# Kernel tuning notes

Hardware: AMD Instinct MI355X
Metric: run time of the kernel (lower is better)

Reference implementation:

```python
import jax, jax.numpy as jnp
import numpy as np

N = 25000   # nodes
E = 600000  # edges (multiple of 48)
IN, H, OUT = 128, 256, 128
SLOPE = 0.01  # LeakyReLU default negative_slope


def _lin(x, w, b):
    return x @ w.T + b


def _leaky(v):
    return jnp.where(v > 0, v, SLOPE * v)


def _sage(x, src, dst, lw, lb, rw):
    # PyG SAGEConv (aggr='mean', root_weight=True, normalize=False):
    # out = lin_l(mean_{j in N(i)} x_j) + lin_r(x_i)
    agg = jax.ops.segment_sum(x[src], dst, num_segments=N)
    deg = jax.ops.segment_sum(jnp.ones((src.shape[0],), x.dtype), dst, num_segments=N)
    mean = agg / jnp.maximum(deg, 1.0)[:, None]
    return mean @ lw.T + lb + x @ rw.T


def setup_inputs() -> dict:
    key = jax.random.key(0)
    ks = jax.random.split(key, 32)

    def w(k, o, i):
        return jax.random.normal(k, (o, i), jnp.float32) * (1.0 / np.sqrt(i))

    def b(k, o):
        return jax.random.normal(k, (o,), jnp.float32) * 0.01

    inp = {
        'x': jax.random.normal(ks[0], (N, IN), jnp.float32),
        'edge_index': jax.random.randint(ks[1], (2, E), 0, N, dtype=jnp.int32),
        'edge_attr': jax.random.normal(ks[2], (E, 1), jnp.float32),
        'batch': jnp.zeros((N,), jnp.int32),
        'prelin_w': w(ks[3], H, IN), 'prelin_b': b(ks[4], H),
        'conv1_lw': w(ks[5], H, H), 'conv1_lb': b(ks[6], H), 'conv1_rw': w(ks[7], H, H),
        'conv2_lw': w(ks[8], H, H), 'conv2_lb': b(ks[9], H), 'conv2_rw': w(ks[10], H, H),
        'conv3_lw': w(ks[11], OUT, H), 'conv3_lb': b(ks[12], OUT), 'conv3_rw': w(ks[13], OUT, H),
        'hh1_w': w(ks[14], H, H), 'hh1_b': b(ks[15], H),
        'hh2_w': w(ks[16], H, H), 'hh2_b': b(ks[17], H),
        'oo_w': w(ks[18], OUT, OUT), 'oo_b': b(ks[19], OUT),
        'lin96_w': w(ks[20], 1, 192), 'lin96_b': b(ks[21], 1),
        'lin32_w': w(ks[22], 1, 64), 'lin32_b': b(ks[23], 1),
    }
    return inp


def reference(x, edge_index, edge_attr, batch,
              prelin_w, prelin_b,
              conv1_lw, conv1_lb, conv1_rw,
              conv2_lw, conv2_lb, conv2_rw,
              conv3_lw, conv3_lb, conv3_rw,
              hh1_w, hh1_b, hh2_w, hh2_b,
              oo_w, oo_b, lin96_w, lin96_b, lin32_w, lin32_b):
    src, dst = edge_index[0], edge_index[1]
    h = jax.nn.relu(_lin(x, prelin_w, prelin_b))
    h = jax.nn.relu(_sage(h, src, dst, conv1_lw, conv1_lb, conv1_rw))
    h = _leaky(_lin(h, hh1_w, hh1_b))
    h = jax.nn.relu(_sage(h, src, dst, conv2_lw, conv2_lb, conv2_rw))
    h = _leaky(_lin(h, hh2_w, hh2_b))
    h = jax.nn.relu(_sage(h, src, dst, conv3_lw, conv3_lb, conv3_rw))
    h = _leaky(_lin(h, oo_w, oo_b))  # [N, 128]

    xl = h[src]  # edge_left  = edge_index[0]
    xr = h[dst]  # edge_right = edge_index[1]
    f96 = jnp.concatenate([xl[:, :96], xr[:, :96]], axis=1)  # [E, 192]
    f32 = jnp.concatenate([xl[:, 96:], xr[:, 96:]], axis=1)  # [E, 64]
    f96 = jax.nn.relu(_lin(f96, lin96_w, lin96_b))  # [E, 1]
    f32 = jax.nn.relu(_lin(f32, lin32_w, lin32_b))  # [E, 1]
    edge_out = f96 * edge_attr + f32                # [E, 1]
    edge_out = edge_out.reshape(-1, 48).mean(axis=1).reshape(-1, 1)  # [E/48, 1]
    return edge_out
```

## Files before the change

kernel.cpp:

```cpp
#include <hip/hip_runtime.h>
#include <hip/hip_bf16.h>

#define N_NODES 25000
#define N_EDGES 600000
#define ACT_NONE 0
#define ACT_RELU 1
#define ACT_LEAKY 2

typedef __bf16 bf16x8 __attribute__((ext_vector_type(8)));
typedef float f32x4 __attribute__((ext_vector_type(4)));
typedef unsigned short u16x8 __attribute__((ext_vector_type(8)));
typedef unsigned short u16x4 __attribute__((ext_vector_type(4)));
typedef short s16x4 __attribute__((ext_vector_type(4)));

__device__ __forceinline__ unsigned short f2bf(float x) {
    union { float f; unsigned int u; } v; v.f = x;
    unsigned int r = (v.u + 0x7fffu + ((v.u >> 16) & 1u)) >> 16;
    return (unsigned short)r;
}
__device__ __forceinline__ float bf2f(unsigned short b) {
    union { float f; unsigned int u; } v; v.u = ((unsigned int)b) << 16;
    return v.f;
}

__global__ __launch_bounds__(256) void hist_kernel(const int* __restrict__ dst,
                                                   int* __restrict__ deg, int E) {
    int e = blockIdx.x * 256 + threadIdx.x;
    if (e < E) atomicAdd(&deg[dst[e]], 1);
}

__global__ __launch_bounds__(1024) void scan_kernel(const int* __restrict__ deg,
                                                    int* __restrict__ off,
                                                    int* __restrict__ cursor, int n) {
    __shared__ int wsum[16];
    int t = threadIdx.x, w = t >> 6, l = t & 63;
    int carry = 0;
    for (int base = 0; base < n; base += 1024) {
        int v = (base + t < n) ? deg[base + t] : 0;
        int x = v;
        #pragma unroll
        for (int d = 1; d < 64; d <<= 1) {
            int y = __shfl_up(x, d);
            if (l >= d) x += y;
        }
        if (l == 63) wsum[w] = x;
        __syncthreads();
        if (w == 0 && l < 16) {
            int s = wsum[l];
            #pragma unroll
            for (int d = 1; d < 16; d <<= 1) {
                int y = __shfl_up(s, d);
                if (l >= d) s += y;
            }
            wsum[l] = s;
        }
        __syncthreads();
        int woff = (w > 0) ? wsum[w - 1] : 0;
        int excl = x + woff - v;
        if (base + t < n) {
            off[base + t] = carry + excl;
            cursor[base + t] = carry + excl;
        }
        int total = wsum[15];
        __syncthreads();
        carry += total;
    }
    if (t == 0) off[n] = carry;
}

__global__ __launch_bounds__(256) void scatter_kernel(const int* __restrict__ src,
                                                      const int* __restrict__ dst,
                                                      int* __restrict__ cursor,
                                                      int* __restrict__ csr_src, int E) {
    int e = blockIdx.x * 256 + threadIdx.x;
    if (e < E) {
        int d = dst[e];
        int pos = atomicAdd(&cursor[d], 1);
        csr_src[pos] = src[e];
    }
}

__global__ __launch_bounds__(256) void convert_kernel(const float* __restrict__ src,
                                                      unsigned short* __restrict__ hi,
                                                      unsigned short* __restrict__ lo, int n) {
    int i = blockIdx.x * 256 + threadIdx.x;
    if (i < n) {
        float x = src[i];
        unsigned short h = f2bf(x);
        hi[i] = h;
        lo[i] = f2bf(x - bf2f(h));
    }
}

struct CvtBatch {
    const float* src[10];
    unsigned short* hi[10];
    unsigned short* lo[10];
    int count[10];
};
__global__ __launch_bounds__(256) void convert_batch_kernel(CvtBatch b) {
    int seg = blockIdx.y;
    int n = b.count[seg];
    int i = blockIdx.x * 256 + threadIdx.x;
    if (i >= n) return;
    float x = b.src[seg][i];
    unsigned short h = f2bf(x);
    b.hi[seg][i] = h;
    b.lo[seg][i] = f2bf(x - bf2f(h));
}

__global__ __launch_bounds__(256) void sage_mean_kernel(const short* __restrict__ qt,
                                                        const float* __restrict__ qs4,
                                                        const int* __restrict__ off,
                                                        const int* __restrict__ csr_src,
                                                        unsigned short* __restrict__ mh,
                                                        unsigned short* __restrict__ ml) {
    int node = blockIdx.x * 4 + (threadIdx.x >> 6);
    if (node >= N_NODES) return;
    int lane = threadIdx.x & 63;
    int qidx = lane >> 4;
    int s0 = off[node], s1 = off[node + 1];
    f32x4 acc0 = {0.f, 0.f, 0.f, 0.f}, acc1 = {0.f, 0.f, 0.f, 0.f};
    f32x4 acc2 = {0.f, 0.f, 0.f, 0.f}, acc3 = {0.f, 0.f, 0.f, 0.f};
    long loff = (long)lane * 4;
    int e = s0;
    for (; e + 4 <= s1; e += 4) {
        int iA = csr_src[e], iB = csr_src[e + 1], iC = csr_src[e + 2], iD = csr_src[e + 3];
        s16x4 qa = *(const s16x4*)&qt[(long)iA * 256 + loff];
        s16x4 qb = *(const s16x4*)&qt[(long)iB * 256 + loff];
        s16x4 qc = *(const s16x4*)&qt[(long)iC * 256 + loff];
        s16x4 qd = *(const s16x4*)&qt[(long)iD * 256 + loff];
        float sa = qs4[(long)iA * 4 + qidx], sb = qs4[(long)iB * 4 + qidx];
        float sc = qs4[(long)iC * 4 + qidx], sd = qs4[(long)iD * 4 + qidx];
        #pragma unroll
        for (int j = 0; j < 4; ++j) {
            acc0[j] += sa * (float)qa[j];
            acc1[j] += sb * (float)qb[j];
            acc2[j] += sc * (float)qc[j];
            acc3[j] += sd * (float)qd[j];
        }
    }
    for (; e < s1; ++e) {
        int iA = csr_src[e];
        s16x4 qa = *(const s16x4*)&qt[(long)iA * 256 + loff];
        float sa = qs4[(long)iA * 4 + qidx];
        #pragma unroll
        for (int j = 0; j < 4; ++j) acc0[j] += sa * (float)qa[j];
    }
    float inv = 1.0f / fmaxf((float)(s1 - s0), 1.0f);
    f32x4 m = ((acc0 + acc1) + (acc2 + acc3)) * inv;
    u16x4 hb, lb;
    #pragma unroll
    for (int j = 0; j < 4; ++j) {
        unsigned short hv = f2bf(m[j]);
        hb[j] = hv;
        lb[j] = f2bf(m[j] - bf2f(hv));
    }
    long base = (long)node * 256 + loff;
    *(u16x4*)&mh[base] = hb;
    *(u16x4*)&ml[base] = lb;
}

__global__ __launch_bounds__(256, 2) void gemm_mfma_kernel(
    const unsigned short* __restrict__ A1h, const unsigned short* __restrict__ A1l,
    const unsigned short* __restrict__ W1h, const unsigned short* __restrict__ W1l,
    const unsigned short* __restrict__ A2h, const unsigned short* __restrict__ A2l,
    const unsigned short* __restrict__ W2h, const unsigned short* __restrict__ W2l,
    const float* __restrict__ bias,
    float* __restrict__ Cf, unsigned short* __restrict__ Ch, unsigned short* __restrict__ Cl,
    short* __restrict__ Cq, float* __restrict__ Cqs,
    const float* __restrict__ w96d, const float* __restrict__ w32d,
    float* __restrict__ nodeDotG,
    int M, int K, int O, int act)
{
    __shared__ unsigned short sAh[128][64];
    __shared__ unsigned short sAl[128][64];
    __shared__ unsigned short sWh[128][64];
    __shared__ unsigned short sWl[128][64];

    int tid = threadIdx.x;
    int row0 = blockIdx.x * 128;
    int col0 = blockIdx.y * 128;
    int wid = tid >> 6, lane = tid & 63;
    int wm = (wid >> 1) * 64, wo = (wid & 1) * 64;
    int fr = lane & 15, qk = lane >> 4;
    int rr = lane >> 3, qq = lane & 7;
    int shalf = (qq >> 2) * 32, scq = qq & 3;

    const int nt1 = K >> 6;
    const int nt  = (A2h != nullptr) ? (nt1 << 1) : nt1;

    f32x4 acc[4][4] = {};

    for (int t = 0; t < nt; ++t) {
        const unsigned short *Ah, *Al, *Wh, *Wl;
        int k0;
        if (t < nt1) { Ah = A1h; Al = A1l; Wh = W1h; Wl = W1l; k0 = t << 6; }
        else         { Ah = A2h; Al = A2l; Wh = W2h; Wl = W2l; k0 = (t - nt1) << 6; }

        #pragma unroll
        for (int i = 0; i < 4; ++i) {
            int rb = wid * 32 + i * 8;
            int r  = rb + rr;
            int gs = shalf + ((scq + (r >> 1)) & 3) * 8;
            long ar = (long)(row0 + r); if (ar > M - 1) ar = M - 1;
            long wr = (long)(col0 + r);
            __builtin_amdgcn_global_load_lds(
                (const __attribute__((address_space(1))) unsigned int*)(Ah + ar * K + k0 + gs),
                (__attribute__((address_space(3))) unsigned int*)&sAh[rb][0], 16, 0, 0);
            __builtin_amdgcn_global_load_lds(
                (const __attribute__((address_space(1))) unsigned int*)(Al + ar * K + k0 + gs),
                (__attribute__((address_space(3))) unsigned int*)&sAl[rb][0], 16, 0, 0);
            __builtin_amdgcn_global_load_lds(
                (const __attribute__((address_space(1))) unsigned int*)(Wh + wr * K + k0 + gs),
                (__attribute__((address_space(3))) unsigned int*)&sWh[rb][0], 16, 0, 0);
            __builtin_amdgcn_global_load_lds(
                (const __attribute__((address_space(1))) unsigned int*)(Wl + wr * K + k0 + gs),
                (__attribute__((address_space(3))) unsigned int*)&sWl[rb][0], 16, 0, 0);
        }
        __syncthreads();

        #pragma unroll
        for (int kk = 0; kk < 2; ++kk) {
            bf16x8 ah[4], al[4], bh[4], bl[4];
            #pragma unroll
            for (int i = 0; i < 4; ++i) {
                int rowA = wm + i * 16 + fr;
                int offA = rowA * 64 + kk * 32 + 8 * ((qk - (rowA >> 1)) & 3);
                ah[i] = *(const bf16x8*)(&sAh[0][0] + offA);
                al[i] = *(const bf16x8*)(&sAl[0][0] + offA);
                int rowB = wo + i * 16 + fr;
                int offB = rowB * 64 + kk * 32 + 8 * ((qk - (rowB >> 1)) & 3);
                bh[i] = *(const bf16x8*)(&sWh[0][0] + offB);
                bl[i] = *(const bf16x8*)(&sWl[0][0] + offB);
            }
            #pragma unroll
            for (int i = 0; i < 4; ++i) {
                #pragma unroll
                for (int j = 0; j < 4; ++j) {
                    acc[i][j] = __builtin_amdgcn_mfma_f32_16x16x32_bf16(ah[i], bh[j], acc[i][j], 0, 0, 0);
                    acc[i][j] = __builtin_amdgcn_mfma_f32_16x16x32_bf16(ah[i], bl[j], acc[i][j], 0, 0, 0);
                    acc[i][j] = __builtin_amdgcn_mfma_f32_16x16x32_bf16(al[i], bh[j], acc[i][j], 0, 0, 0);
                }
            }
        }
        __syncthreads();
    }

    int rgrp = (lane >> 4) * 4;
    int cl_ = lane & 15;
    int quarter = (col0 + wo) >> 6;

    float wa96[4], wb96[4], wa32[4], wb32[4];
    if (nodeDotG) {
        #pragma unroll
        for (int j = 0; j < 4; ++j) {
            int c = wo + j * 16 + cl_;
            bool lo96 = c < 96;
            wa96[j] = lo96 ? w96d[c] : 0.0f;
            wb96[j] = lo96 ? w96d[96 + c] : 0.0f;
            wa32[j] = lo96 ? 0.0f : w32d[c - 96];
            wb32[j] = lo96 ? 0.0f : w32d[c - 64];
        }
    }

    #pragma unroll
    for (int i = 0; i < 4; ++i) {
        float bv[4];
        #pragma unroll
        for (int j = 0; j < 4; ++j) bv[j] = bias[col0 + wo + j * 16 + cl_];
        #pragma unroll
        for (int r = 0; r < 4; ++r) {
            int grow = row0 + wm + i * 16 + rgrp + r;
            float vv[4];
            float m = 0.0f;
            #pragma unroll
            for (int j = 0; j < 4; ++j) {
                float v = acc[i][j][r] + bv[j];
                if (act == ACT_RELU)       v = fmaxf(v, 0.0f);
                else if (act == ACT_LEAKY) v = (v > 0.0f) ? v : 0.01f * v;
                vv[j] = v;
                m = fmaxf(m, fabsf(v));
            }
            float qinv = 0.0f;
            if (Cq) {
                #pragma unroll
                for (int d = 1; d < 16; d <<= 1) m = fmaxf(m, __shfl_xor(m, d));
                qinv = (m > 0.0f) ? 32767.0f / m : 0.0f;
            }
            bool ok = grow < M;
            #pragma unroll
            for (int j = 0; j < 4; ++j) {
                int gcol = col0 + wo + j * 16 + cl_;
                long idx = (long)grow * O + gcol;
                if (ok) {
                    float v = vv[j];
                    if (Cf) Cf[idx] = v;
                    if (Ch) {
                        unsigned short hbits = f2bf(v);
                        Ch[idx] = hbits;
                        Cl[idx] = f2bf(v - bf2f(hbits));
                    }
                    if (Cq) Cq[idx] = (short)(int)rintf(v * qinv);
                }
            }
            if (Cq && ok && cl_ == 0)
                Cqs[(long)grow * 4 + quarter] = (m > 0.0f) ? m / 32767.0f : 0.0f;

            if (nodeDotG) {
                float pL96 = vv[0]*wa96[0] + vv[1]*wa96[1] + vv[2]*wa96[2] + vv[3]*wa96[3];
                float pR96 = vv[0]*wb96[0] + vv[1]*wb96[1] + vv[2]*wb96[2] + vv[3]*wb96[3];
                float pL32 = vv[0]*wa32[0] + vv[1]*wa32[1] + vv[2]*wa32[2] + vv[3]*wa32[3];
                float pR32 = vv[0]*wb32[0] + vv[1]*wb32[1] + vv[2]*wb32[2] + vv[3]*wb32[3];
                #pragma unroll
                for (int d = 1; d < 16; d <<= 1) {
                    pL96 += __shfl_xor(pL96, d);
                    pR96 += __shfl_xor(pR96, d);
                    pL32 += __shfl_xor(pL32, d);
                    pR32 += __shfl_xor(pR32, d);
                }
                if (cl_ == 0) {
                    int rl = wm + i * 16 + rgrp + r;
                    f32x4 pv = {pL96, pR96, pL32, pR32};
                    ((f32x4*)&sAh[0][0])[rl * 2 + (wo >> 6)] = pv;
                }
            }
        }
    }

    if (nodeDotG) {
        __syncthreads();
        if (wo == 0) {
            int rl = wm + lane;
            int grow = row0 + rl;
            if (grow < M) {
                f32x4 a = ((f32x4*)&sAh[0][0])[rl * 2 + 0];
                f32x4 b = ((f32x4*)&sAh[0][0])[rl * 2 + 1];
                f32x4 s = a + b;
                *(f32x4*)&nodeDotG[(long)grow * 4] = s;
            }
        }
    }
}

__global__ __launch_bounds__(256) void edge_group_kernel(const float* __restrict__ nodeDot,
                                                         const int* __restrict__ src,
                                                         const int* __restrict__ dst,
                                                         const float* __restrict__ eattr,
                                                         const float* __restrict__ b96,
                                                         const float* __restrict__ b32,
                                                         float* __restrict__ out, int G) {
    int g = blockIdx.x * 256 + threadIdx.x;
    if (g >= G) return;
    float bb96 = b96[0], bb32 = b32[0];
    int base = g * 48;
    float s = 0.0f;
    #pragma unroll 4
    for (int k = 0; k < 48; ++k) {
        int e = base + k;
        f32x4 a = *(const f32x4*)&nodeDot[(long)src[e] * 4];
        f32x4 b = *(const f32x4*)&nodeDot[(long)dst[e] * 4];
        float f96  = fmaxf(a[0] + b[1] + bb96, 0.0f);
        float f32v = fmaxf(a[2] + b[3] + bb32, 0.0f);
        s += f96 * eattr[e] + f32v;
    }
    out[g] = s * (1.0f / 48.0f);
}

extern "C" void kernel_launch(void* const* d_in, const int* in_sizes, int n_in,
                              void* d_out, int out_size, void* d_ws, size_t ws_size,
                              hipStream_t stream) {
    const float* x         = (const float*)d_in[0];
    const int*   edge_idx  = (const int*)d_in[1];
    const float* edge_attr = (const float*)d_in[2];
    const float* prelin_w  = (const float*)d_in[4];
    const float* prelin_b  = (const float*)d_in[5];
    const float* conv1_lw  = (const float*)d_in[6];
    const float* conv1_lb  = (const float*)d_in[7];
    const float* conv1_rw  = (const float*)d_in[8];
    const float* conv2_lw  = (const float*)d_in[9];
    const float* conv2_lb  = (const float*)d_in[10];
    const float* conv2_rw  = (const float*)d_in[11];
    const float* conv3_lw  = (const float*)d_in[12];
    const float* conv3_lb  = (const float*)d_in[13];
    const float* conv3_rw  = (const float*)d_in[14];
    const float* hh1_w     = (const float*)d_in[15];
    const float* hh1_b     = (const float*)d_in[16];
    const float* hh2_w     = (const float*)d_in[17];
    const float* hh2_b     = (const float*)d_in[18];
    const float* oo_w      = (const float*)d_in[19];
    const float* oo_b      = (const float*)d_in[20];
    const float* lin96_w   = (const float*)d_in[21];
    const float* lin96_b   = (const float*)d_in[22];
    const float* lin32_w   = (const float*)d_in[23];
    const float* lin32_b   = (const float*)d_in[24];

    const int* src = edge_idx;
    const int* dst = edge_idx + N_EDGES;

    char* wsp = (char*)d_ws;
    size_t used = 0;
    auto alloc = [&](size_t bytes) -> char* {
        char* r = wsp;
        size_t pad = (bytes + 255) & ~(size_t)255;
        wsp += pad; used += pad;
        return r;
    };
    unsigned short* P0h = (unsigned short*)alloc((size_t)N_NODES * 256 * 2);
    unsigned short* P0l = (unsigned short*)alloc((size_t)N_NODES * 256 * 2);
    unsigned short* P1h = (unsigned short*)alloc((size_t)N_NODES * 256 * 2);
    unsigned short* P1l = (unsigned short*)alloc((size_t)N_NODES * 256 * 2);
    unsigned short* P2h = (unsigned short*)alloc((size_t)N_NODES * 256 * 2);
    unsigned short* P2l = (unsigned short*)alloc((size_t)N_NODES * 256 * 2);
    short* qtab    = (short*)alloc((size_t)N_NODES * 256 * 2);
    float* qsc4    = (float*)alloc((size_t)N_NODES * 4 * 4);
    float* nodeDot = (float*)alloc((size_t)N_NODES * 4 * 4);
    int* deg       = (int*)alloc((size_t)N_NODES * 4);
    int* off       = (int*)alloc((size_t)(N_NODES + 1) * 4);
    int* cursor    = (int*)alloc((size_t)N_NODES * 4);
    int* csr_src   = (int*)alloc((size_t)N_EDGES * 4);

    struct WP { unsigned short *h, *l; };
    auto wpair = [&](int n) -> WP {
        WP w; w.h = (unsigned short*)alloc((size_t)n * 2);
        w.l = (unsigned short*)alloc((size_t)n * 2); return w;
    };
    WP w_pre = wpair(256 * 128);
    WP w_c1l = wpair(256 * 256), w_c1r = wpair(256 * 256);
    WP w_c2l = wpair(256 * 256), w_c2r = wpair(256 * 256);
    WP w_c3l = wpair(128 * 256), w_c3r = wpair(128 * 256);
    WP w_h1  = wpair(256 * 256), w_h2 = wpair(256 * 256);
    WP w_oo  = wpair(128 * 128);

    if (used > ws_size) return;

    const int EB = (N_EDGES + 255) / 256;
    const int MB = (N_NODES + 127) / 128;
    const int NB4 = (N_NODES + 3) / 4;

    (void)hipMemsetAsync(deg, 0, N_NODES * sizeof(int), stream);
    hist_kernel<<<EB, 256, 0, stream>>>(dst, deg, N_EDGES);
    scan_kernel<<<1, 1024, 0, stream>>>(deg, off, cursor, N_NODES);
    scatter_kernel<<<EB, 256, 0, stream>>>(src, dst, cursor, csr_src, N_EDGES);

    convert_kernel<<<((N_NODES * 128) + 255) / 256, 256, 0, stream>>>(x, P0h, P0l, N_NODES * 128);
    CvtBatch cb;
    const float* wsrc[10] = {prelin_w, conv1_lw, conv1_rw, conv2_lw, conv2_rw,
                             conv3_lw, conv3_rw, hh1_w, hh2_w, oo_w};
    WP wdst[10] = {w_pre, w_c1l, w_c1r, w_c2l, w_c2r, w_c3l, w_c3r, w_h1, w_h2, w_oo};
    int wcnt[10] = {256 * 128, 256 * 256, 256 * 256, 256 * 256, 256 * 256,
                    128 * 256, 128 * 256, 256 * 256, 256 * 256, 128 * 128};
    for (int i = 0; i < 10; ++i) {
        cb.src[i] = wsrc[i]; cb.hi[i] = wdst[i].h; cb.lo[i] = wdst[i].l; cb.count[i] = wcnt[i];
    }
    convert_batch_kernel<<<dim3((65536 + 255) / 256, 10), 256, 0, stream>>>(cb);

    gemm_mfma_kernel<<<dim3(MB, 2), 256, 0, stream>>>(
        P0h, P0l, w_pre.h, w_pre.l, nullptr, nullptr, nullptr, nullptr,
        prelin_b, nullptr, P1h, P1l, qtab, qsc4,
        nullptr, nullptr, nullptr, N_NODES, 128, 256, ACT_RELU);

    sage_mean_kernel<<<NB4, 256, 0, stream>>>(qtab, qsc4, off, csr_src, P2h, P2l);
    gemm_mfma_kernel<<<dim3(MB, 2), 256, 0, stream>>>(
        P2h, P2l, w_c1l.h, w_c1l.l, P1h, P1l, w_c1r.h, w_c1r.l,
        conv1_lb, nullptr, P0h, P0l, nullptr, nullptr,
        nullptr, nullptr, nullptr, N_NODES, 256, 256, ACT_RELU);
    gemm_mfma_kernel<<<dim3(MB, 2), 256, 0, stream>>>(
        P0h, P0l, w_h1.h, w_h1.l, nullptr, nullptr, nullptr, nullptr,
        hh1_b, nullptr, P1h, P1l, qtab, qsc4,
        nullptr, nullptr, nullptr, N_NODES, 256, 256, ACT_LEAKY);

    sage_mean_kernel<<<NB4, 256, 0, stream>>>(qtab, qsc4, off, csr_src, P2h, P2l);
    gemm_mfma_kernel<<<dim3(MB, 2), 256, 0, stream>>>(
        P2h, P2l, w_c2l.h, w_c2l.l, P1h, P1l, w_c2r.h, w_c2r.l,
        conv2_lb, nullptr, P0h, P0l, nullptr, nullptr,
        nullptr, nullptr, nullptr, N_NODES, 256, 256, ACT_RELU);
    gemm_mfma_kernel<<<dim3(MB, 2), 256, 0, stream>>>(
        P0h, P0l, w_h2.h, w_h2.l, nullptr, nullptr, nullptr, nullptr,
        hh2_b, nullptr, P1h, P1l, qtab, qsc4,
        nullptr, nullptr, nullptr, N_NODES, 256, 256, ACT_LEAKY);

    sage_mean_kernel<<<NB4, 256, 0, stream>>>(qtab, qsc4, off, csr_src, P2h, P2l);
    gemm_mfma_kernel<<<dim3(MB, 1), 256, 0, stream>>>(
        P2h, P2l, w_c3l.h, w_c3l.l, P1h, P1l, w_c3r.h, w_c3r.l,
        conv3_lb, nullptr, P0h, P0l, nullptr, nullptr,
        nullptr, nullptr, nullptr, N_NODES, 256, 128, ACT_RELU);
    gemm_mfma_kernel<<<dim3(MB, 1), 256, 0, stream>>>(
        P0h, P0l, w_oo.h, w_oo.l, nullptr, nullptr, nullptr, nullptr,
        oo_b, nullptr, nullptr, nullptr, nullptr, nullptr,
        lin96_w, lin32_w, nodeDot, N_NODES, 128, 128, ACT_LEAKY);

    const int G = N_EDGES / 48;
    edge_group_kernel<<<(G + 255) / 256, 256, 0, stream>>>(
        nodeDot, src, dst, edge_attr, lin96_b, lin32_b, (float*)d_out, G);
}
```

Measured before the change: 440.9 us.

## Split sage mean aggregation into column slices with 8 lanes per node

The mean-aggregation kernel now gives each node 8 threads covering one 32-column slice, and the block index encodes which of the 8 column slices it handles. Consecutive blocks in a chunk touch the same node neighbourhoods but different columns, so the gathered qtab rows should be shared in L2 and each wavefront handles 8 nodes at once. This exposes more independent gather streams per wave and narrows per-node load imbalance. In exchange, the CSR index and scale reads are repeated across the 8 slices and the edge loop is unrolled only by two.

```diff
diff --git a/kernel.cpp b/kernel.cpp
--- a/kernel.cpp
+++ b/kernel.cpp
@@ -115,40 +115,37 @@
                                                         const int* __restrict__ csr_src,
                                                         unsigned short* __restrict__ mh,
                                                         unsigned short* __restrict__ ml) {
-    int node = blockIdx.x * 4 + (threadIdx.x >> 6);
+    int slice = blockIdx.x & 7;
+    int chunk = blockIdx.x >> 3;
+    int g = threadIdx.x >> 3;
+    int l = threadIdx.x & 7;
+    int node = chunk * 32 + g;
     if (node >= N_NODES) return;
-    int lane = threadIdx.x & 63;
-    int qidx = lane >> 4;
+    int qq = slice >> 1;
+    long colbase = slice * 32 + l * 4;
     int s0 = off[node], s1 = off[node + 1];
     f32x4 acc0 = {0.f, 0.f, 0.f, 0.f}, acc1 = {0.f, 0.f, 0.f, 0.f};
-    f32x4 acc2 = {0.f, 0.f, 0.f, 0.f}, acc3 = {0.f, 0.f, 0.f, 0.f};
-    long loff = (long)lane * 4;
     int e = s0;
-    for (; e + 4 <= s1; e += 4) {
-        int iA = csr_src[e], iB = csr_src[e + 1], iC = csr_src[e + 2], iD = csr_src[e + 3];
-        s16x4 qa = *(const s16x4*)&qt[(long)iA * 256 + loff];
-        s16x4 qb = *(const s16x4*)&qt[(long)iB * 256 + loff];
-        s16x4 qc = *(const s16x4*)&qt[(long)iC * 256 + loff];
-        s16x4 qd = *(const s16x4*)&qt[(long)iD * 256 + loff];
-        float sa = qs4[(long)iA * 4 + qidx], sb = qs4[(long)iB * 4 + qidx];
-        float sc = qs4[(long)iC * 4 + qidx], sd = qs4[(long)iD * 4 + qidx];
+    for (; e + 2 <= s1; e += 2) {
+        int iA = csr_src[e], iB = csr_src[e + 1];
+        s16x4 qa = *(const s16x4*)&qt[(long)iA * 256 + colbase];
+        s16x4 qb = *(const s16x4*)&qt[(long)iB * 256 + colbase];
+        float sa = qs4[(long)iA * 4 + qq], sb = qs4[(long)iB * 4 + qq];
         #pragma unroll
         for (int j = 0; j < 4; ++j) {
             acc0[j] += sa * (float)qa[j];
             acc1[j] += sb * (float)qb[j];
-            acc2[j] += sc * (float)qc[j];
-            acc3[j] += sd * (float)qd[j];
-        }
-    }
-    for (; e < s1; ++e) {
+        }
+    }
+    if (e < s1) {
         int iA = csr_src[e];
-        s16x4 qa = *(const s16x4*)&qt[(long)iA * 256 + loff];
-        float sa = qs4[(long)iA * 4 + qidx];
+        s16x4 qa = *(const s16x4*)&qt[(long)iA * 256 + colbase];
+        float sa = qs4[(long)iA * 4 + qq];
         #pragma unroll
         for (int j = 0; j < 4; ++j) acc0[j] += sa * (float)qa[j];
     }
     float inv = 1.0f / fmaxf((float)(s1 - s0), 1.0f);
-    f32x4 m = ((acc0 + acc1) + (acc2 + acc3)) * inv;
+    f32x4 m = (acc0 + acc1) * inv;
     u16x4 hb, lb;
     #pragma unroll
     for (int j = 0; j < 4; ++j) {
@@ -156,7 +153,7 @@
         hb[j] = hv;
         lb[j] = f2bf(m[j] - bf2f(hv));
     }
-    long base = (long)node * 256 + loff;
+    long base = (long)node * 256 + colbase;
     *(u16x4*)&mh[base] = hb;
     *(u16x4*)&ml[base] = lb;
 }
@@ -436,7 +433,7 @@
 
     const int EB = (N_EDGES + 255) / 256;
     const int MB = (N_NODES + 127) / 128;
-    const int NB4 = (N_NODES + 3) / 4;
+    const int NBS = 8 * ((N_NODES + 31) / 32);
 
     (void)hipMemsetAsync(deg, 0, N_NODES * sizeof(int), stream);
     hist_kernel<<<EB, 256, 0, stream>>>(dst, deg, N_EDGES);
@@ -460,7 +457,7 @@
         prelin_b, nullptr, P1h, P1l, qtab, qsc4,
         nullptr, nullptr, nullptr, N_NODES, 128, 256, ACT_RELU);
 
-    sage_mean_kernel<<<NB4, 256, 0, stream>>>(qtab, qsc4, off, csr_src, P2h, P2l);
+    sage_mean_kernel<<<NBS, 256, 0, stream>>>(qtab, qsc4, off, csr_src, P2h, P2l);
     gemm_mfma_kernel<<<dim3(MB, 2), 256, 0, stream>>>(
         P2h, P2l, w_c1l.h, w_c1l.l, P1h, P1l, w_c1r.h, w_c1r.l,
         conv1_lb, nullptr, P0h, P0l, nullptr, nullptr,
@@ -470,7 +467,7 @@
         hh1_b, nullptr, P1h, P1l, qtab, qsc4,
         nullptr, nullptr, nullptr, N_NODES, 256, 256, ACT_LEAKY);
 
-    sage_mean_kernel<<<NB4, 256, 0, stream>>>(qtab, qsc4, off, csr_src, P2h, P2l);
+    sage_mean_kernel<<<NBS, 256, 0, stream>>>(qtab, qsc4, off, csr_src, P2h, P2l);
     gemm_mfma_kernel<<<dim3(MB, 2), 256, 0, stream>>>(
         P2h, P2l, w_c2l.h, w_c2l.l, P1h, P1l, w_c2r.h, w_c2r.l,
         conv2_lb, nullptr, P0h, P0l, nullptr, nullptr,
@@ -480,7 +477,7 @@
         hh2_b, nullptr, P1h, P1l, qtab, qsc4,
         nullptr, nullptr, nullptr, N_NODES, 256, 256, ACT_LEAKY);
 
-    sage_mean_kernel<<<NB4, 256, 0, stream>>>(qtab, qsc4, off, csr_src, P2h, P2l);
+    sage_mean_kernel<<<NBS, 256, 0, stream>>>(qtab, qsc4, off, csr_src, P2h, P2l);
     gemm_mfma_kernel<<<dim3(MB, 1), 256, 0, stream>>>(
         P2h, P2l, w_c3l.h, w_c3l.l, P1h, P1l, w_c3r.h, w_c3r.l,
         conv3_lb, nullptr, P0h, P0l, nullptr, nullptr,
```

Result: slower. 536.8 us (+21.7%).
